# Kernel tuning notes

Measured on AMD Instinct MI355X. Metric: run time of the kernel, lower is better.

The kernel has to match this reference:

```python
import jax, jax.numpy as jnp
import numpy as np


def _ln(z, g, b, eps=1e-5):
    mu = z.mean(-1, keepdims=True)
    v = ((z - mu) ** 2).mean(-1, keepdims=True)
    return (z - mu) / jnp.sqrt(v + eps) * g + b


def _forward(x, C_prev, n_prev, m_prev, ln_in_g, ln_in_b, wq, bq, wk, bk, wv, bv, wi, bi, wf, bf, wo, bo, rd_w1, rd_b1, rd_g, rd_be, rd_w2, rd_b2, ssm_log_lam, ssm_log_b, ssm_c, ssm_log_d, ssm_log_step, ssm_vol_gate, ssm_alpha, ssm_ln_g, ssm_ln_b, ln_mem_g, ln_mem_b):
    B, S, F = x.shape
    D = wq.shape[0]
    sqd = jnp.sqrt(jnp.float32(D))
    w = max(1, int(S * 0.2))
    pad0 = jnp.zeros((B, 1, F), x.dtype)
    cs = jnp.concatenate([pad0, jnp.cumsum(x, 1)], 1)
    cs2 = jnp.concatenate([pad0, jnp.cumsum(x * x, 1)], 1)
    wsum = cs[:, w:] - cs[:, :-w]
    wsq = cs2[:, w:] - cs2[:, :-w]
    var = (wsq - wsum * wsum / w) / (w - 1)
    std = jnp.sqrt(jnp.clip(var, 0.0))
    vol = jnp.concatenate([jnp.broadcast_to(std[:, :1], (B, w - 1, F)), std], 1)
    sv = vol.mean(2, keepdims=True)
    sv = sv / (sv.mean(1, keepdims=True) + 1e-6)  # [B,S,1]
    # --- parallel gate computation ---
    xn = _ln(x, ln_in_g, ln_in_b)
    regime = jax.nn.softmax(jax.nn.gelu(_ln(xn @ rd_w1.T + rd_b1, rd_g, rd_be), approximate=False) @ rd_w2.T + rd_b2, axis=-1)
    q = xn @ wq.T + bq
    k = (xn @ wk.T + bk) / sqd
    v = xn @ wv.T + bv
    it = xn @ wi.T + bi  # [B,S,1]
    ft = xn @ wf.T + bf
    o = jax.nn.sigmoid(xn @ wo.T + bo)
    # --- stabilize_gates (running-max exponential stabilization) ---
    mp = jnp.clip(m_prev, -100.0, 100.0)[:, None, :]  # [B,1,1]
    m_t = jnp.maximum(ft, mp + ft)
    ig = jnp.exp(jnp.clip(it - m_t, -15.0, 15.0))
    fg = jnp.exp(jnp.clip(ft + mp - m_t, -15.0, 15.0))
    # --- store_key_value outer products + cumulative matrix memory ---
    kn = k / (jnp.linalg.norm(k, axis=2, keepdims=True) + 1e-12) * sqd
    vn = v / (jnp.linalg.norm(v, axis=2, keepdims=True) + 1e-6) * sqd
    upd = jnp.clip(ig, 0.0, 1.0)[..., None] * (vn[..., :, None] * kn[..., None, :])  # [B,S,D,D]
    f_cum = jnp.cumprod(fg, axis=1)  # [B,S,1]
    C_t = f_cum[..., None] * C_prev[:, None] + jnp.cumsum(upd, 1)
    # --- structured state-space mixing, vectorized over the D memory rows ---
    lam = -jnp.exp(ssm_log_lam)
    step = jnp.exp(ssm_log_step)
    a_disc = (2.0 + step * lam) / (2.0 - step * lam)  # bilinear discretization
    b_disc = step * (1.0 + a_disc) * jnp.exp(ssm_log_b)[:, 0] / 2.0
    xr = C_t.transpose(0, 2, 1, 3).reshape(B * D, S, D)  # rows folded into batch
    volr = jnp.broadcast_to(sv[:, None, :, 0], (B, D, S)).reshape(B * D, S)
    u = xr.mean(-1)  # [BD,S], per-step scalar drive
    vgate = jax.nn.sigmoid(ssm_vol_gate)
    def stepf(h, inp):
        u_t, vol_t = inp
        h = a_disc[None] * h + b_disc[None] * u_t[:, None]
        h = _ln(h, ssm_ln_g, ssm_ln_b)
        h = h / (1.0 + vgate[None] * vol_t[:, None])
        return h, h
    h0 = jnp.zeros((B * D, D), x.dtype)
    _, hs = jax.lax.scan(stepf, h0, (u.T, volr.T))  # [S,BD,D]
    yscal = jnp.einsum('sbn,n->bs', hs, ssm_c[0])  # [BD,S]
    y = yscal[..., None] + jnp.exp(ssm_log_d) * xr
    alpha = jax.nn.sigmoid(ssm_alpha)
    mixed = alpha * xr + (1.0 - alpha) * y
    C_mixed = mixed.reshape(B, D, S, D).transpose(0, 2, 1, 3)
    mf = regime[:, :, 0:1][..., None]  # regime-aware mixing factor
    C_t = C_mixed * mf + C_t * (1.0 - mf)
    C_t = C_t / (jnp.linalg.norm(C_t.reshape(B, S, D * D), axis=-1)[..., None, None] + 1e-6) * sqd
    # --- mLSTM readout (stabilizer_threshold = 1.0) ---
    n_t = f_cum * n_prev[:, None, :] + jnp.cumsum(ig * k, 1)
    h_til = jnp.einsum('bsij,bsj->bsi', C_t, q)
    denom = jnp.maximum(jnp.abs(jnp.sum(n_t * q, -1, keepdims=True)), 1.0)
    return o * _ln(h_til / denom, ln_mem_g, ln_mem_b)


def setup_inputs() -> dict:
    key = jax.random.key(0)
    ks = jax.random.split(key, 12)
    B, S, F, D = 8, 512, 32, 64
    sF, sD = 1.0 / np.sqrt(F), 1.0 / np.sqrt(D)
    n = lambda k, sh, s=1.0: jax.random.normal(k, sh, jnp.float32) * s
    return dict(
        x=n(ks[0], (B, S, F)),
        C_prev=jnp.zeros((B, D, D), jnp.float32),
        n_prev=jnp.zeros((B, D), jnp.float32),
        m_prev=jnp.zeros((B, 1), jnp.float32),
        ln_in_g=jnp.ones((F,), jnp.float32), ln_in_b=jnp.zeros((F,), jnp.float32),
        wq=n(ks[1], (D, F), sF), bq=jnp.zeros((D,), jnp.float32),
        wk=n(ks[2], (D, F), sF), bk=jnp.zeros((D,), jnp.float32),
        wv=n(ks[3], (D, F), sF), bv=jnp.zeros((D,), jnp.float32),
        wi=n(ks[4], (1, F), sF), bi=jnp.zeros((1,), jnp.float32),
        wf=n(ks[5], (1, F), sF), bf=jnp.ones((1,), jnp.float32),
        wo=n(ks[6], (D, F), sF), bo=jnp.zeros((D,), jnp.float32),
        rd_w1=n(ks[7], (D, F), sF), rd_b1=jnp.zeros((D,), jnp.float32),
        rd_g=jnp.ones((D,), jnp.float32), rd_be=jnp.zeros((D,), jnp.float32),
        rd_w2=n(ks[8], (4, D), sD), rd_b2=jnp.zeros((4,), jnp.float32),
        ssm_log_lam=jnp.linspace(np.log(0.001), np.log(0.1), D).astype(jnp.float32),
        ssm_log_b=jax.random.uniform(ks[9], (D, 1), jnp.float32, -0.5, 0.5),
        ssm_c=n(ks[10], (1, D), sD),
        ssm_log_d=jnp.zeros((1,), jnp.float32),
        ssm_log_step=jnp.float32(np.log(0.001)),
        ssm_vol_gate=jnp.ones((D,), jnp.float32),
        ssm_alpha=jnp.float32(0.7),
        ssm_ln_g=jnp.ones((D,), jnp.float32), ssm_ln_b=jnp.zeros((D,), jnp.float32),
        ln_mem_g=jnp.ones((D,), jnp.float32), ln_mem_b=jnp.zeros((D,), jnp.float32),
    )


def reference(x, C_prev, n_prev, m_prev, ln_in_g, ln_in_b, wq, bq, wk, bk, wv, bv, wi, bi, wf, bf, wo, bo, rd_w1, rd_b1, rd_g, rd_be, rd_w2, rd_b2, ssm_log_lam, ssm_log_b, ssm_c, ssm_log_d, ssm_log_step, ssm_vol_gate, ssm_alpha, ssm_ln_g, ssm_ln_b, ln_mem_g, ln_mem_b):
    return _forward(x, C_prev, n_prev, m_prev, ln_in_g, ln_in_b, wq, bq, wk, bk, wv, bv, wi, bi, wf, bf, wo, bo, rd_w1, rd_b1, rd_g, rd_be, rd_w2, rd_b2, ssm_log_lam, ssm_log_b, ssm_c, ssm_log_d, ssm_log_step, ssm_vol_gate, ssm_alpha, ssm_ln_g, ssm_ln_b, ln_mem_g, ln_mem_b)
```

## Files before the change

### kernel.cpp

```cpp
#include <hip/hip_runtime.h>
#include <math.h>

#define BB 8
#define SS 512
#define FF 32
#define DD 64
#define WVOL 102
#define CH 16
#define NCH (SS / CH)

template<int CTRL, int RM, bool BC>
__device__ __forceinline__ float updpp(float oldv, float x) {
  return __int_as_float(__builtin_amdgcn_update_dpp(
      __float_as_int(oldv), __float_as_int(x), CTRL, RM, 0xF, BC));
}
__device__ __forceinline__ float rlane(float v, int l) {
  return __int_as_float(__builtin_amdgcn_readlane(__float_as_int(v), l));
}
__device__ __forceinline__ float dsum64(float x) {
  x += updpp<0x111, 0xF, true>(0.f, x);
  x += updpp<0x112, 0xF, true>(0.f, x);
  x += updpp<0x114, 0xF, true>(0.f, x);
  x += updpp<0x118, 0xF, true>(0.f, x);
  x += updpp<0x142, 0xF, true>(0.f, x);
  x += updpp<0x143, 0xF, true>(0.f, x);
  return rlane(x, 63);
}
__device__ __forceinline__ void dred2(float& a, float& b) {
  a += updpp<0x111,0xF,true>(0.f,a); b += updpp<0x111,0xF,true>(0.f,b);
  a += updpp<0x112,0xF,true>(0.f,a); b += updpp<0x112,0xF,true>(0.f,b);
  a += updpp<0x114,0xF,true>(0.f,a); b += updpp<0x114,0xF,true>(0.f,b);
  a += updpp<0x118,0xF,true>(0.f,a); b += updpp<0x118,0xF,true>(0.f,b);
  a += updpp<0x142,0xF,true>(0.f,a); b += updpp<0x142,0xF,true>(0.f,b);
  a += updpp<0x143,0xF,true>(0.f,a); b += updpp<0x143,0xF,true>(0.f,b);
  a = rlane(a, 63); b = rlane(b, 63);
}
__device__ __forceinline__ void dred3(float& a, float& b, float& c) {
  a += updpp<0x111,0xF,true>(0.f,a); b += updpp<0x111,0xF,true>(0.f,b); c += updpp<0x111,0xF,true>(0.f,c);
  a += updpp<0x112,0xF,true>(0.f,a); b += updpp<0x112,0xF,true>(0.f,b); c += updpp<0x112,0xF,true>(0.f,c);
  a += updpp<0x114,0xF,true>(0.f,a); b += updpp<0x114,0xF,true>(0.f,b); c += updpp<0x114,0xF,true>(0.f,c);
  a += updpp<0x118,0xF,true>(0.f,a); b += updpp<0x118,0xF,true>(0.f,b); c += updpp<0x118,0xF,true>(0.f,c);
  a += updpp<0x142,0xF,true>(0.f,a); b += updpp<0x142,0xF,true>(0.f,b); c += updpp<0x142,0xF,true>(0.f,c);
  a += updpp<0x143,0xF,true>(0.f,a); b += updpp<0x143,0xF,true>(0.f,b); c += updpp<0x143,0xF,true>(0.f,c);
  a = rlane(a, 63); b = rlane(b, 63); c = rlane(c, 63);
}
__device__ __forceinline__ void dred4(float& a, float& b, float& c, float& d) {
  a += updpp<0x111,0xF,true>(0.f,a); b += updpp<0x111,0xF,true>(0.f,b); c += updpp<0x111,0xF,true>(0.f,c); d += updpp<0x111,0xF,true>(0.f,d);
  a += updpp<0x112,0xF,true>(0.f,a); b += updpp<0x112,0xF,true>(0.f,b); c += updpp<0x112,0xF,true>(0.f,c); d += updpp<0x112,0xF,true>(0.f,d);
  a += updpp<0x114,0xF,true>(0.f,a); b += updpp<0x114,0xF,true>(0.f,b); c += updpp<0x114,0xF,true>(0.f,c); d += updpp<0x114,0xF,true>(0.f,d);
  a += updpp<0x118,0xF,true>(0.f,a); b += updpp<0x118,0xF,true>(0.f,b); c += updpp<0x118,0xF,true>(0.f,c); d += updpp<0x118,0xF,true>(0.f,d);
  a += updpp<0x142,0xF,true>(0.f,a); b += updpp<0x142,0xF,true>(0.f,b); c += updpp<0x142,0xF,true>(0.f,c); d += updpp<0x142,0xF,true>(0.f,d);
  a += updpp<0x143,0xF,true>(0.f,a); b += updpp<0x143,0xF,true>(0.f,b); c += updpp<0x143,0xF,true>(0.f,c); d += updpp<0x143,0xF,true>(0.f,d);
  a = rlane(a, 63); b = rlane(b, 63); c = rlane(c, 63); d = rlane(d, 63);
}
__device__ __forceinline__ void dred2_32(float& a, float& b) {
  a += updpp<0x111,0xF,true>(0.f,a); b += updpp<0x111,0xF,true>(0.f,b);
  a += updpp<0x112,0xF,true>(0.f,a); b += updpp<0x112,0xF,true>(0.f,b);
  a += updpp<0x114,0xF,true>(0.f,a); b += updpp<0x114,0xF,true>(0.f,b);
  a += updpp<0x118,0xF,true>(0.f,a); b += updpp<0x118,0xF,true>(0.f,b);
  a += updpp<0x142,0xF,true>(0.f,a); b += updpp<0x142,0xF,true>(0.f,b);
  a = rlane(a, 31); b = rlane(b, 31);
}
__device__ __forceinline__ float dsum16(float x) {
  x += updpp<0x111, 0xF, true>(0.f, x);
  x += updpp<0x112, 0xF, true>(0.f, x);
  x += updpp<0x114, 0xF, true>(0.f, x);
  x += updpp<0x118, 0xF, true>(0.f, x);
  return x;
}
__device__ __forceinline__ void dscan3(float& f, float& z, float& r) {
  f *= updpp<0x111,0xF,false>(1.f,f); z += updpp<0x111,0xF,true>(0.f,z); r += updpp<0x111,0xF,true>(0.f,r);
  f *= updpp<0x112,0xF,false>(1.f,f); z += updpp<0x112,0xF,true>(0.f,z); r += updpp<0x112,0xF,true>(0.f,r);
  f *= updpp<0x114,0xF,false>(1.f,f); z += updpp<0x114,0xF,true>(0.f,z); r += updpp<0x114,0xF,true>(0.f,r);
  f *= updpp<0x118,0xF,false>(1.f,f); z += updpp<0x118,0xF,true>(0.f,z); r += updpp<0x118,0xF,true>(0.f,r);
  f *= updpp<0x142,0xA,false>(1.f,f); z += updpp<0x142,0xA,true>(0.f,z); r += updpp<0x142,0xA,true>(0.f,r);
  f *= updpp<0x143,0xC,false>(1.f,f); z += updpp<0x143,0xC,true>(0.f,z); r += updpp<0x143,0xC,true>(0.f,r);
}

__global__ void k_prep(const float* __restrict__ Cp,
                       const float* __restrict__ wq, const float* __restrict__ wk,
                       const float* __restrict__ wv, const float* __restrict__ wo,
                       const float* __restrict__ rw1,
                       float* __restrict__ CpT, float* __restrict__ wqT,
                       float* __restrict__ wkT, float* __restrict__ wvT,
                       float* __restrict__ woT, float* __restrict__ rw1T,
                       float* __restrict__ cpr, float* __restrict__ cpn2) {
  int blk = blockIdx.x; int lane = threadIdx.x;
  if (blk < BB) {
    int b = blk;
    const float* rowp = Cp + (size_t)(b * DD + lane) * DD;
    float rs = 0.f, r2 = 0.f;
#pragma unroll 8
    for (int j = 0; j < DD; ++j) {
      float c = rowp[j];
      rs += c; r2 = fmaf(c, c, r2);
      CpT[(size_t)(b * DD + j) * DD + lane] = c;
    }
    cpr[b * DD + lane] = rs;
    float tot2 = dsum64(r2);
    if (lane == 0) cpn2[b] = tot2;
  } else {
    const float* src; float* dst;
    switch (blk - BB) {
      case 0: src = wq;  dst = wqT;  break;
      case 1: src = wk;  dst = wkT;  break;
      case 2: src = wv;  dst = wvT;  break;
      case 3: src = wo;  dst = woT;  break;
      default: src = rw1; dst = rw1T; break;
    }
#pragma unroll 8
    for (int f = 0; f < FF; ++f) dst[f * DD + lane] = src[lane * FF + f];
  }
}

__global__ void k_vol_std(const float* __restrict__ x, float* __restrict__ svraw) {
  int b = blockIdx.x; int s = WVOL - 1 + blockIdx.y;
  int lane = threadIdx.x; int f = lane & 31; int half = lane >> 5;
  const float* xb = x + (size_t)(b * SS) * FF + f;
  float wsum = 0.f, wsq = 0.f;
  int t0 = s - WVOL + 1 + half;
#pragma unroll 17
  for (int k = 0; k < WVOL / 2; ++k) {
    float xv = xb[(t0 + 2 * k) * FF];
    wsum += xv; wsq = fmaf(xv, xv, wsq);
  }
  wsum += __shfl_xor(wsum, 32); wsq += __shfl_xor(wsq, 32);
  float var = (wsq - wsum * wsum * (1.f / WVOL)) * (1.f / (WVOL - 1));
  float sd = sqrtf(fmaxf(var, 0.f));
  float m = dsum64(sd) * 0.5f * (1.f / FF);
  if (lane == 0) svraw[b * SS + s] = m;
}

__global__ void k_proj(const float* __restrict__ x, const float* __restrict__ m_prev,
                       const float* __restrict__ CpT,
                       const float* __restrict__ ln_in_g, const float* __restrict__ ln_in_b,
                       const float* __restrict__ wqT, const float* __restrict__ bq,
                       const float* __restrict__ wkT, const float* __restrict__ bk,
                       const float* __restrict__ wvT, const float* __restrict__ bv,
                       const float* __restrict__ wi, const float* __restrict__ bi,
                       const float* __restrict__ wf, const float* __restrict__ bf,
                       const float* __restrict__ woT, const float* __restrict__ bo,
                       const float* __restrict__ rw1T, const float* __restrict__ rd_b1,
                       const float* __restrict__ rd_g, const float* __restrict__ rd_be,
                       const float* __restrict__ rd_w2, const float* __restrict__ rd_b2,
                       float* __restrict__ qo, float* __restrict__ kno, float* __restrict__ vno,
                       float* __restrict__ iko, float* __restrict__ oo,
                       float* __restrict__ cg_a, float* __restrict__ fg_a,
                       float* __restrict__ mf_a, float* __restrict__ cks_a,
                       float* __restrict__ qsum_a, float* __restrict__ zc) {
  int bs = blockIdx.x; int b = bs / SS;
  int lane = threadIdx.x;
  __shared__ float xs[FF];
  __shared__ float ks[DD];
  float xv = (lane < FF) ? x[bs * FF + lane] : 0.f;
  float s1x = xv, s2x = xv * xv;
  dred2_32(s1x, s2x);
  if (lane < FF) {
    float mu = s1x * (1.f / FF);
    float var = s2x * (1.f / FF) - mu * mu;
    xs[lane] = (xv - mu) * rsqrtf(var + 1e-5f) * ln_in_g[lane] + ln_in_b[lane];
  }
  __syncthreads();
  int d = lane;
  float aq = bq[d], ak = bk[d], av = bv[d], ao = bo[d], at = rd_b1[d];
#pragma unroll
  for (int f = 0; f < FF; ++f) {
    float xf = xs[f];
    aq = fmaf(xf, wqT[f * DD + d], aq);
    ak = fmaf(xf, wkT[f * DD + d], ak);
    av = fmaf(xf, wvT[f * DD + d], av);
    ao = fmaf(xf, woT[f * DD + d], ao);
    at = fmaf(xf, rw1T[f * DD + d], at);
  }
  float pit = (lane < FF) ? xs[lane] * wi[lane] : 0.f;
  float pft = (lane < FF) ? xs[lane] * wf[lane] : 0.f;
  dred2_32(pit, pft);
  float itv = pit + bi[0];
  float ftv = pft + bf[0];
  float s1 = at, s2 = at * at;
  dred2(s1, s2);
  float mu = s1 * (1.f / DD);
  float var = s2 * (1.f / DD) - mu * mu;
  float tn = (at - mu) * rsqrtf(var + 1e-5f) * rd_g[d] + rd_be[d];
  float ge = 0.5f * tn * (1.f + erff(tn * 0.70710678118654752f));
  float l0 = ge * rd_w2[0 * DD + d], l1 = ge * rd_w2[1 * DD + d];
  float l2 = ge * rd_w2[2 * DD + d], l3 = ge * rd_w2[3 * DD + d];
  dred4(l0, l1, l2, l3);
  l0 += rd_b2[0]; l1 += rd_b2[1]; l2 += rd_b2[2]; l3 += rd_b2[3];
  float mx = fmaxf(fmaxf(l0, l1), fmaxf(l2, l3));
  float e0 = expf(l0 - mx), e1 = expf(l1 - mx), e2 = expf(l2 - mx), e3 = expf(l3 - mx);
  float mfv = e0 / (e0 + e1 + e2 + e3);
  float kd = ak * 0.125f;
  float kk = kd * kd, vv = av * av, qsum = aq;
  dred3(kk, vv, qsum);
  float knd = kd * (8.f / (sqrtf(kk) + 1e-12f));
  float vnd = av * (8.f / (sqrtf(vv) + 1e-6f));
  float ksum = dsum64(knd);
  float mp = fminf(fmaxf(m_prev[b], -100.f), 100.f);
  float mt = fmaxf(ftv, mp + ftv);
  float ig = expf(fminf(fmaxf(itv - mt, -15.f), 15.f));
  float fg = expf(fminf(fmaxf(ftv + mp - mt, -15.f), 15.f));
  float cg = fminf(ig, 1.f);
  qo[bs * DD + d] = aq;
  kno[bs * DD + d] = knd;
  vno[bs * DD + d] = vnd;
  iko[bs * DD + d] = ig * kd;
  oo[bs * DD + d] = 1.f / (1.f + expf(-ao));
  ks[d] = knd;
  __syncthreads();
  float acc = 0.f;
  const float* cpt = CpT + (size_t)b * DD * DD;
#pragma unroll 8
  for (int j = 0; j < DD; ++j) acc = fmaf(cpt[j * DD + d], ks[j], acc);
  float z = dsum64(vnd * acc);
  if (lane == 0) {
    cg_a[bs] = cg; fg_a[bs] = fg; mf_a[bs] = mfv;
    cks_a[bs] = cg * ksum; qsum_a[bs] = qsum;
    zc[bs] = cg * z;
  }
}

__global__ void k_qk(const float* __restrict__ qo, const float* __restrict__ kno,
                     const float* __restrict__ vno, const float* __restrict__ cg_a,
                     float* __restrict__ W, float* __restrict__ rho) {
  int blk = blockIdx.x; int b = blk / 136; int r = blk % 136;
  int st = 0;
  while ((st + 1) * (st + 2) / 2 <= r) ++st;
  int tt = r - st * (st + 1) / 2;
  int s0 = st * 32, t0 = tt * 32;
  int tid = threadIdx.x; int ty = tid >> 4, tx = tid & 15;
  __shared__ float qls[32][64], kls[32][64], vsl[32][64];
  __shared__ float ktl[32][68], vtl[32][68];
  __shared__ float cgl[32], sacc[32];
  {
    int col = tid & 63, rg = tid >> 6;
#pragma unroll
    for (int rr = 0; rr < 8; ++rr) {
      int row = rg * 8 + rr;
      int gi = (b * SS + s0 + row) * DD + col;
      int gj = (b * SS + t0 + row) * DD + col;
      qls[row][col] = qo[gi]; kls[row][col] = kno[gi]; vsl[row][col] = vno[gi];
      ktl[row][col] = kno[gj]; vtl[row][col] = vno[gj];
    }
    if (tid < 32) cgl[tid] = cg_a[b * SS + t0 + tid];
  }
  __syncthreads();
  float A[2][2] = {{0.f, 0.f}, {0.f, 0.f}};
  float KK[2][2] = {{0.f, 0.f}, {0.f, 0.f}};
  float VV[2][2] = {{0.f, 0.f}, {0.f, 0.f}};
  for (int k4 = 0; k4 < DD; k4 += 4) {
    float qa[2][4], ka[2][4], va[2][4], kt[2][4], vt[2][4];
#pragma unroll
    for (int i = 0; i < 2; ++i) {
      float4 t1 = *(const float4*)&qls[ty * 2 + i][k4];
      qa[i][0] = t1.x; qa[i][1] = t1.y; qa[i][2] = t1.z; qa[i][3] = t1.w;
      float4 t2 = *(const float4*)&kls[ty * 2 + i][k4];
      ka[i][0] = t2.x; ka[i][1] = t2.y; ka[i][2] = t2.z; ka[i][3] = t2.w;
      float4 t3 = *(const float4*)&vsl[ty * 2 + i][k4];
      va[i][0] = t3.x; va[i][1] = t3.y; va[i][2] = t3.z; va[i][3] = t3.w;
      float4 t4 = *(const float4*)&ktl[tx * 2 + i][k4];
      kt[i][0] = t4.x; kt[i][1] = t4.y; kt[i][2] = t4.z; kt[i][3] = t4.w;
      float4 t5 = *(const float4*)&vtl[tx * 2 + i][k4];
      vt[i][0] = t5.x; vt[i][1] = t5.y; vt[i][2] = t5.z; vt[i][3] = t5.w;
    }
#pragma unroll
    for (int kk = 0; kk < 4; ++kk)
#pragma unroll
      for (int i = 0; i < 2; ++i)
#pragma unroll
        for (int j = 0; j < 2; ++j) {
          A[i][j]  = fmaf(qa[i][kk], kt[j][kk], A[i][j]);
          KK[i][j] = fmaf(ka[i][kk], kt[j][kk], KK[i][j]);
          VV[i][j] = fmaf(va[i][kk], vt[j][kk], VV[i][j]);
        }
  }
  float cg0 = cgl[tx * 2], cg1 = cgl[tx * 2 + 1];
  int tg0 = t0 + tx * 2, tg1 = t0 + tx * 2 + 1;
#pragma unroll
  for (int i = 0; i < 2; ++i) {
    int s = s0 + ty * 2 + i;
    float w0 = (tg0 <= s) ? cg0 * A[i][0] : 0.f;
    float w1 = (tg1 <= s) ? cg1 * A[i][1] : 0.f;
    float2 wst = make_float2(w0, w1);
    *(float2*)&W[((size_t)b * SS + s) * SS + tg0] = wst;
    float wr0 = (tg0 < s) ? 2.f : (tg0 == s ? 1.f : 0.f);
    float wr1 = (tg1 < s) ? 2.f : (tg1 == s ? 1.f : 0.f);
    float rsum = dsum16(fmaf(wr0 * cg0, KK[i][0] * VV[i][0],
                             wr1 * cg1 * KK[i][1] * VV[i][1]));
    if (tx == 15) sacc[ty * 2 + i] = rsum;
  }
  __syncthreads();
  if (tid < 32) {
    int s = s0 + tid;
    atomicAdd(&rho[b * SS + s], cg_a[b * SS + s] * sacc[tid]);
  }
}

__global__ void k_pv(const float* __restrict__ W, const float* __restrict__ vno,
                     float* __restrict__ p2) {
  int blk = blockIdx.x; int b = blk / 26; int u = blk % 26;
  int st32, c0, c1;
  if (u < 6) { st32 = u; c0 = 0; c1 = u >> 1; }
  else {
    int v = u - 6; st32 = 6 + (v >> 1);
    int nch = (st32 >> 1) + 1; int h0 = nch >> 1;
    if (v & 1) { c0 = h0; c1 = nch - 1; } else { c0 = 0; c1 = h0 - 1; }
  }
  int s0 = st32 * 32;
  int tid = threadIdx.x; int ty = tid >> 4, tx = tid & 15;
  __shared__ float wls[32][64];
  __shared__ float vls[64][64];
  float acc[2][4] = {{0.f, 0.f, 0.f, 0.f}, {0.f, 0.f, 0.f, 0.f}};
  for (int c = c0; c <= c1; ++c) {
    __syncthreads();
    int t0 = c * 64;
    int col = tid & 63, rg = tid >> 6;
#pragma unroll
    for (int rr = 0; rr < 8; ++rr) {
      int r2 = rg * 8 + rr;
      wls[r2][col] = W[((size_t)b * SS + s0 + r2) * SS + t0 + col];
    }
#pragma unroll
    for (int rr = 0; rr < 16; ++rr) {
      int t = rg * 16 + rr;
      vls[t][col] = vno[(b * SS + t0 + t) * DD + col];
    }
    __syncthreads();
    for (int k4 = 0; k4 < 64; k4 += 4) {
      float aa[2][4];
#pragma unroll
      for (int i = 0; i < 2; ++i) {
        float4 t1 = *(const float4*)&wls[ty * 2 + i][k4];
        aa[i][0] = t1.x; aa[i][1] = t1.y; aa[i][2] = t1.z; aa[i][3] = t1.w;
      }
      float bb[4][4];
#pragma unroll
      for (int kk = 0; kk < 4; ++kk) {
        float4 t2 = *(const float4*)&vls[k4 + kk][tx * 4];
        bb[kk][0] = t2.x; bb[kk][1] = t2.y; bb[kk][2] = t2.z; bb[kk][3] = t2.w;
      }
#pragma unroll
      for (int kk = 0; kk < 4; ++kk)
#pragma unroll
        for (int i = 0; i < 2; ++i)
#pragma unroll
          for (int j = 0; j < 4; ++j)
            acc[i][j] = fmaf(aa[i][kk], bb[kk][j], acc[i][j]);
    }
  }
#pragma unroll
  for (int i = 0; i < 2; ++i)
#pragma unroll
    for (int j = 0; j < 4; ++j)
      atomicAdd(&p2[(b * SS + s0 + ty * 2 + i) * DD + tx * 4 + j], acc[i][j]);
}

__global__ void k_post(const float* __restrict__ fg_a, const float* __restrict__ zc,
                       const float* __restrict__ rho, const float* __restrict__ svraw,
                       const float* __restrict__ ik, const float* __restrict__ vno,
                       const float* __restrict__ cks_a,
                       float* __restrict__ fcum, float* __restrict__ cpd,
                       float* __restrict__ sn2, float* __restrict__ sv,
                       float* __restrict__ csn, float* __restrict__ csr) {
  int blk = blockIdx.x; int lane = threadIdx.x;
  if (blk < BB) {
    int b = blk;
    float m0 = svraw[b * SS + WVOL - 1];
    float vals[8]; float part = 0.f;
#pragma unroll
    for (int c = 0; c < 8; ++c) {
      int idx = c * 64 + lane;
      float v = (idx < WVOL - 1) ? m0 : svraw[b * SS + idx];
      vals[c] = v; part += v;
    }
    float tot = dsum64(part);
    float inv = 1.f / (tot * (1.f / SS) + 1e-6f);
#pragma unroll
    for (int c = 0; c < 8; ++c) sv[b * SS + c * 64 + lane] = vals[c] * inv;
    float cf = 1.f, cz = 0.f, crr = 0.f;
    for (int c = 0; c < 8; ++c) {
      int bs = b * SS + c * 64 + lane;
      float f = fg_a[bs], z = zc[bs], r = rho[bs];
      dscan3(f, z, r);
      f *= cf; z += cz; r += crr;
      fcum[bs] = f; cpd[bs] = z; sn2[bs] = r;
      cf = rlane(f, 63); cz = rlane(z, 63); crr = rlane(r, 63);
    }
  } else {
    int blk2 = blk - BB; int b = blk2 / NCH; int w = blk2 % NCH; int d = lane;
    float na = 0.f, ra = 0.f;
#pragma unroll
    for (int t = 0; t < CH; ++t) {
      int bs = b * SS + w * CH + t;
      na += ik[bs * DD + d];
      ra = fmaf(cks_a[bs], vno[bs * DD + d], ra);
    }
    csn[blk2 * DD + d] = na; csr[blk2 * DD + d] = ra;
  }
}

__global__ void k_scan_apply(const float* __restrict__ ik, const float* __restrict__ vno,
                             const float* __restrict__ cks_a,
                             const float* __restrict__ csn, const float* __restrict__ csr,
                             const float* __restrict__ sv,
                             const float* __restrict__ cvec, const float* __restrict__ ln_g,
                             const float* __restrict__ ln_b, const float* __restrict__ vol_gate,
                             float* __restrict__ nacc, float* __restrict__ racc,
                             float* __restrict__ S1g, float* __restrict__ S2g) {
  int blk = blockIdx.x;
  if (blk < BB * NCH) {
    int b = blk / NCH; int w = blk % NCH; int d = threadIdx.x;
    float na = 0.f, ra = 0.f;
    for (int w2 = 0; w2 < w; ++w2) {
      na += csn[(b * NCH + w2) * DD + d];
      ra += csr[(b * NCH + w2) * DD + d];
    }
#pragma unroll
    for (int t = 0; t < CH; ++t) {
      int bs = b * SS + w * CH + t;
      na += ik[bs * DD + d];
      ra = fmaf(cks_a[bs], vno[bs * DD + d], ra);
      nacc[bs * DD + d] = na;
      racc[bs * DD + d] = ra;
    }
  } else {
    int bs = blk - BB * NCH;
    int nn = threadIdx.x;
    float cn = cvec[nn], g = ln_g[nn], be = ln_b[nn];
    float vg = 1.f / (1.f + expf(-vol_gate[nn]));
    float vol = sv[bs];
    float rden = __builtin_amdgcn_rcpf(fmaf(vg, vol, 1.f));
    float r1 = cn * g * rden, r2 = cn * be * rden;
    dred2(r1, r2);
    if (nn == 0) { S1g[bs] = r1; S2g[bs] = r2; }
  }
}

__global__ void k_ssm(const float* __restrict__ fcum, const float* __restrict__ racc,
                      const float* __restrict__ cpr, const float* __restrict__ sv,
                      const float* __restrict__ log_lam, const float* __restrict__ log_b,
                      const float* __restrict__ cvec,
                      const float* __restrict__ log_step, const float* __restrict__ vol_gate,
                      const float* __restrict__ ln_g, const float* __restrict__ ln_b,
                      const float* __restrict__ S1g, const float* __restrict__ S2g,
                      float* __restrict__ ysT) {
  int blk = blockIdx.x; int b = blk >> 6; int i = blk & 63;
  int n = threadIdx.x;
  float st = expf(log_step[0]);
  float lam = -expf(log_lam[n]);
  float ad = (2.f + st * lam) / (2.f - st * lam);
  float bd = st * (1.f + ad) * expf(log_b[n]) * 0.5f;
  float vg = 1.f / (1.f + expf(-vol_gate[n]));
  float g = ln_g[n], be = ln_b[n], cn = cvec[n];
  float adg = ad * g, adbe = ad * be, cng = cn * g;
  float cprv = cpr[b * DD + i];
  float u[8], w[8], S1a[8], S2a[8];
#pragma unroll
  for (int c = 0; c < 8; ++c) {
    int s = c * 64 + n; int bs = b * SS + s;
    u[c] = fmaf(fcum[bs], cprv, racc[(size_t)bs * DD + i]) * (1.f / DD);
    w[c] = sv[bs];
    S1a[c] = S1g[bs]; S2a[c] = S2g[bs];
  }
  float ht = bd * rlane(u[0], 0);
#pragma unroll
  for (int c = 0; c < 8; ++c) {
    float macc = 0.f, iacc = 0.f, s3acc = 0.f;
#pragma unroll 4
    for (int t2 = 0; t2 < 64; ++t2) {
      float vvol = rlane(w[c], t2);
      float rden = __builtin_amdgcn_rcpf(fmaf(vg, vvol, 1.f));
      float p1 = ht, p2 = ht * ht, p3 = (cng * rden) * ht;
      p1 += updpp<0x111,0xF,true>(0.f,p1); p2 += updpp<0x111,0xF,true>(0.f,p2); p3 += updpp<0x111,0xF,true>(0.f,p3);
      p1 += updpp<0x112,0xF,true>(0.f,p1); p2 += updpp<0x112,0xF,true>(0.f,p2); p3 += updpp<0x112,0xF,true>(0.f,p3);
      p1 += updpp<0x114,0xF,true>(0.f,p1); p2 += updpp<0x114,0xF,true>(0.f,p2); p3 += updpp<0x114,0xF,true>(0.f,p3);
      p1 += updpp<0x118,0xF,true>(0.f,p1); p2 += updpp<0x118,0xF,true>(0.f,p2); p3 += updpp<0x118,0xF,true>(0.f,p3);
      p1 += updpp<0x142,0xF,true>(0.f,p1); p2 += updpp<0x142,0xF,true>(0.f,p2); p3 += updpp<0x142,0xF,true>(0.f,p3);
      p1 += updpp<0x143,0xF,true>(0.f,p1); p2 += updpp<0x143,0xF,true>(0.f,p2); p3 += updpp<0x143,0xF,true>(0.f,p3);
      float s1 = rlane(p1, 63), s2v = rlane(p2, 63), s3 = rlane(p3, 63);
      float mu = s1 * (1.f / DD);
      float r2m = fmaf(-mu, s1, s2v);
      float arg = fmaxf(fmaf(r2m, 1.f / DD, 1e-5f), 1e-5f);
      float irs = __builtin_amdgcn_rsqf(arg);
      bool sel = (n == t2);
      macc = sel ? mu : macc;
      iacc = sel ? irs : iacc;
      s3acc = sel ? s3 : s3acc;
      float un = (t2 < 63) ? rlane(u[c], t2 + 1)
                           : ((c < 7) ? rlane(u[(c + 1) & 7], 0) : 0.f);
      float A = adg * rden;
      float B = fmaf(adbe, rden, bd * un);
      ht = fmaf((ht - mu) * A, irs, B);
    }
    float y = fmaf(iacc, fmaf(-macc, S1a[c], s3acc), S2a[c]);
    ysT[(size_t)(b * DD + i) * SS + c * 64 + n] = y;
  }
}

__global__ void k_final(const float* __restrict__ qo, const float* __restrict__ oo,
                        const float* __restrict__ p2, const float* __restrict__ racc,
                        const float* __restrict__ nacc, const float* __restrict__ ysT,
                        const float* __restrict__ CpT, const float* __restrict__ cpr,
                        const float* __restrict__ cpn2,
                        const float* __restrict__ fcum, const float* __restrict__ cpd,
                        const float* __restrict__ sn2,
                        const float* __restrict__ mf_a, const float* __restrict__ qsum_a,
                        const float* __restrict__ n_prev,
                        const float* __restrict__ ssm_log_d, const float* __restrict__ ssm_alpha,
                        const float* __restrict__ ln_mem_g, const float* __restrict__ ln_mem_b,
                        float* __restrict__ out) {
  int bs = blockIdx.x; int b = bs / SS; int s = bs % SS;
  int i = threadIdx.x;
  __shared__ float qv[DD];
  float qi = qo[bs * DD + i];
  qv[i] = qi;
  __syncthreads();
  float P1 = 0.f;
  const float* cpt = CpT + (size_t)b * DD * DD;
#pragma unroll 8
  for (int j = 0; j < DD; ++j) P1 = fmaf(cpt[j * DD + i], qv[j], P1);
  float fc = fcum[bs];
  float p = fmaf(fc, P1, p2[bs * DD + i]);
  float r = fmaf(fc, cpr[b * DD + i], racc[bs * DD + i]);
  float R2 = fc * fc * cpn2[b] + 2.f * fc * cpd[bs] + sn2[bs];
  float al = 1.f / (1.f + expf(-ssm_alpha[0]));
  float kap = al + (1.f - al) * expf(ssm_log_d[0]);
  float mfv = mf_a[bs];
  float beta = 1.f + mfv * (kap - 1.f);
  float gam = mfv * (1.f - al);
  float y = ysT[(size_t)(b * DD + i) * SS + s];
  float nt = fmaf(fc, n_prev[b * DD + i], nacc[bs * DD + i]);
  float syr = y * r, sy2 = y * y, ndp = nt * qi;
  dred3(syr, sy2, ndp);
  float nrm2 = fmaxf(beta * beta * R2 + 2.f * beta * gam * syr + gam * gam * (float)DD * sy2, 0.f);
  float scale = 8.f / (sqrtf(nrm2) + 1e-6f);
  float denom = fmaxf(fabsf(ndp), 1.f);
  float hh = scale * (fmaf(beta, p, gam * y * qsum_a[bs])) / denom;
  float s1 = hh, s2 = hh * hh;
  dred2(s1, s2);
  float mu = s1 * (1.f / DD);
  float var = fmaxf(s2 * (1.f / DD) - mu * mu, 0.f);
  float o = (hh - mu) * rsqrtf(var + 1e-5f) * ln_mem_g[i] + ln_mem_b[i];
  out[bs * DD + i] = oo[bs * DD + i] * o;
}

extern "C" void kernel_launch(void* const* d_in, const int* in_sizes, int n_in,
                              void* d_out, int out_size, void* d_ws, size_t ws_size,
                              hipStream_t stream) {
  const float* x        = (const float*)d_in[0];
  const float* C_prev   = (const float*)d_in[1];
  const float* n_prev   = (const float*)d_in[2];
  const float* m_prev   = (const float*)d_in[3];
  const float* ln_in_g  = (const float*)d_in[4];
  const float* ln_in_b  = (const float*)d_in[5];
  const float* wq = (const float*)d_in[6];  const float* bq = (const float*)d_in[7];
  const float* wk = (const float*)d_in[8];  const float* bk = (const float*)d_in[9];
  const float* wv = (const float*)d_in[10]; const float* bv = (const float*)d_in[11];
  const float* wi = (const float*)d_in[12]; const float* bi = (const float*)d_in[13];
  const float* wf = (const float*)d_in[14]; const float* bf = (const float*)d_in[15];
  const float* wo = (const float*)d_in[16]; const float* bo = (const float*)d_in[17];
  const float* rd_w1 = (const float*)d_in[18]; const float* rd_b1 = (const float*)d_in[19];
  const float* rd_g  = (const float*)d_in[20]; const float* rd_be = (const float*)d_in[21];
  const float* rd_w2 = (const float*)d_in[22]; const float* rd_b2 = (const float*)d_in[23];
  const float* ssm_log_lam  = (const float*)d_in[24];
  const float* ssm_log_b    = (const float*)d_in[25];
  const float* ssm_c        = (const float*)d_in[26];
  const float* ssm_log_d    = (const float*)d_in[27];
  const float* ssm_log_step = (const float*)d_in[28];
  const float* ssm_vol_gate = (const float*)d_in[29];
  const float* ssm_alpha    = (const float*)d_in[30];
  const float* ssm_ln_g     = (const float*)d_in[31];
  const float* ssm_ln_b     = (const float*)d_in[32];
  const float* ln_mem_g     = (const float*)d_in[33];
  const float* ln_mem_b     = (const float*)d_in[34];
  float* out = (float*)d_out;

  float* Wsp = (float*)d_ws;
  size_t o0 = 0;
  const size_t BS = (size_t)BB * SS, BSD = BS * DD, WSZ = (size_t)BB * SS * SS;
  float* sv    = Wsp + o0; o0 += BS;
  float* svraw = Wsp + o0; o0 += BS;
  float* qo   = Wsp + o0; o0 += BSD;
  float* kno  = Wsp + o0; o0 += BSD;
  float* vno  = Wsp + o0; o0 += BSD;
  float* iko  = Wsp + o0; o0 += BSD;
  float* oo   = Wsp + o0; o0 += BSD;
  float* racc = Wsp + o0; o0 += BSD;
  float* nacc = Wsp + o0; o0 += BSD;
  float* ysT  = Wsp + o0; o0 += BSD;
  float* p2   = Wsp + o0; o0 += BSD;
  float* rho  = Wsp + o0; o0 += BS;
  float* Wm   = Wsp + o0; o0 += WSZ;
  float* cg_a = Wsp + o0; o0 += BS;
  float* fg_a = Wsp + o0; o0 += BS;
  float* mf_a = Wsp + o0; o0 += BS;
  float* cks  = Wsp + o0; o0 += BS;
  float* qsum = Wsp + o0; o0 += BS;
  float* zc   = Wsp + o0; o0 += BS;
  float* fcum = Wsp + o0; o0 += BS;
  float* cpd  = Wsp + o0; o0 += BS;
  float* sn2  = Wsp + o0; o0 += BS;
  float* S1g  = Wsp + o0; o0 += BS;
  float* S2g  = Wsp + o0; o0 += BS;
  float* cpr  = Wsp + o0; o0 += (size_t)BB * DD;
  float* cpn2 = Wsp + o0; o0 += BB;
  float* csn  = Wsp + o0; o0 += (size_t)BB * NCH * DD;
  float* csr  = Wsp + o0; o0 += (size_t)BB * NCH * DD;
  float* CpT  = Wsp + o0; o0 += (size_t)BB * DD * DD;
  float* wqT  = Wsp + o0; o0 += (size_t)FF * DD;
  float* wkT  = Wsp + o0; o0 += (size_t)FF * DD;
  float* wvT  = Wsp + o0; o0 += (size_t)FF * DD;
  float* woT  = Wsp + o0; o0 += (size_t)FF * DD;
  float* rw1T = Wsp + o0; o0 += (size_t)FF * DD;

  hipMemsetAsync(p2, 0, (BSD + BS + WSZ) * sizeof(float), stream);
  hipLaunchKernelGGL(k_prep, dim3(BB + 5), dim3(64), 0, stream,
                     C_prev, wq, wk, wv, wo, rd_w1,
                     CpT, wqT, wkT, wvT, woT, rw1T, cpr, cpn2);
  hipLaunchKernelGGL(k_vol_std, dim3(BB, SS - WVOL + 1), dim3(64), 0, stream, x, svraw);
  hipLaunchKernelGGL(k_proj, dim3(BB * SS), dim3(64), 0, stream,
                     x, m_prev, CpT, ln_in_g, ln_in_b, wqT, bq, wkT, bk, wvT, bv, wi, bi,
                     wf, bf, woT, bo, rw1T, rd_b1, rd_g, rd_be, rd_w2, rd_b2,
                     qo, kno, vno, iko, oo, cg_a, fg_a, mf_a, cks, qsum, zc);
  hipLaunchKernelGGL(k_qk, dim3(BB * 136), dim3(256), 0, stream,
                     qo, kno, vno, cg_a, Wm, rho);
  hipLaunchKernelGGL(k_pv, dim3(BB * 26), dim3(256), 0, stream, Wm, vno, p2);
  hipLaunchKernelGGL(k_post, dim3(BB + BB * NCH), dim3(64), 0, stream,
                     fg_a, zc, rho, svraw, iko, vno, cks,
                     fcum, cpd, sn2, sv, csn, csr);
  hipLaunchKernelGGL(k_scan_apply, dim3(BB * NCH + BB * SS), dim3(64), 0, stream,
                     iko, vno, cks, csn, csr, sv, ssm_c, ssm_ln_g, ssm_ln_b,
                     ssm_vol_gate, nacc, racc, S1g, S2g);
  hipLaunchKernelGGL(k_ssm, dim3(BB * DD), dim3(64), 0, stream,
                     fcum, racc, cpr, sv, ssm_log_lam, ssm_log_b, ssm_c,
                     ssm_log_step, ssm_vol_gate, ssm_ln_g, ssm_ln_b, S1g, S2g, ysT);
  hipLaunchKernelGGL(k_final, dim3(BB * SS), dim3(64), 0, stream,
                     qo, oo, p2, racc, nacc, ysT, CpT, cpr, cpn2, fcum, cpd, sn2,
                     mf_a, qsum, n_prev, ssm_log_d, ssm_alpha, ln_mem_g, ln_mem_b, out);
}
```

Measured before the change: 300.4 us.

## Pack four SSM rows per wave and precompute per-step gate coefficients

The SSM scan kernel now processes four memory rows per 64-lane wave, with 16 lanes per row and four state elements per lane. The per-step LayerNorm reductions therefore need only four in-row DPP steps instead of a full-wave reduction plus readlanes. The per-step volatility-dependent coefficients (ad*g/rden, ad*be/rden, c*g/rden) are precomputed in the scan_apply kernel into three new B×S×D buffers. The scan reads them as float4, prefetched one step ahead. This shortens the serial dependency chain per step and raises per-lane ILP. In exchange it launches a quarter as many waves, adds global traffic for the coefficient buffers, and puts dependent global loads inside the sequential loop.

```diff
diff --git a/kernel.cpp b/kernel.cpp
--- a/kernel.cpp
+++ b/kernel.cpp
@@ -405,8 +405,11 @@
                              const float* __restrict__ sv,
                              const float* __restrict__ cvec, const float* __restrict__ ln_g,
                              const float* __restrict__ ln_b, const float* __restrict__ vol_gate,
+                             const float* __restrict__ log_lam, const float* __restrict__ log_step,
                              float* __restrict__ nacc, float* __restrict__ racc,
-                             float* __restrict__ S1g, float* __restrict__ S2g) {
+                             float* __restrict__ S1g, float* __restrict__ S2g,
+                             float* __restrict__ AdgR, float* __restrict__ AbeR,
+                             float* __restrict__ CngR) {
   int blk = blockIdx.x;
   if (blk < BB * NCH) {
     int b = blk / NCH; int w = blk % NCH; int d = threadIdx.x;
@@ -428,72 +431,128 @@
     int nn = threadIdx.x;
     float cn = cvec[nn], g = ln_g[nn], be = ln_b[nn];
     float vg = 1.f / (1.f + expf(-vol_gate[nn]));
+    float st = expf(log_step[0]);
+    float lam = -expf(log_lam[nn]);
+    float ad = (2.f + st * lam) / (2.f - st * lam);
     float vol = sv[bs];
     float rden = __builtin_amdgcn_rcpf(fmaf(vg, vol, 1.f));
-    float r1 = cn * g * rden, r2 = cn * be * rden;
+    float cgr = cn * g * rden;
+    AdgR[(size_t)bs * DD + nn] = ad * g * rden;
+    AbeR[(size_t)bs * DD + nn] = ad * be * rden;
+    CngR[(size_t)bs * DD + nn] = cgr;
+    float r1 = cgr, r2 = cn * be * rden;
     dred2(r1, r2);
     if (nn == 0) { S1g[bs] = r1; S2g[bs] = r2; }
   }
 }
 
 __global__ void k_ssm(const float* __restrict__ fcum, const float* __restrict__ racc,
-                      const float* __restrict__ cpr, const float* __restrict__ sv,
+                      const float* __restrict__ cpr,
+                      const float* __restrict__ AdgR, const float* __restrict__ AbeR,
+                      const float* __restrict__ CngR,
+                      const float* __restrict__ S1g, const float* __restrict__ S2g,
                       const float* __restrict__ log_lam, const float* __restrict__ log_b,
-                      const float* __restrict__ cvec,
-                      const float* __restrict__ log_step, const float* __restrict__ vol_gate,
-                      const float* __restrict__ ln_g, const float* __restrict__ ln_b,
-                      const float* __restrict__ S1g, const float* __restrict__ S2g,
+                      const float* __restrict__ log_step,
                       float* __restrict__ ysT) {
-  int blk = blockIdx.x; int b = blk >> 6; int i = blk & 63;
-  int n = threadIdx.x;
+  int w = blockIdx.x;
+  int b = w >> 4;
+  int ig = (w & 15) << 2;
+  int lane = threadIdx.x;
+  int n16 = lane & 15, row = lane >> 4;
   float st = expf(log_step[0]);
-  float lam = -expf(log_lam[n]);
-  float ad = (2.f + st * lam) / (2.f - st * lam);
-  float bd = st * (1.f + ad) * expf(log_b[n]) * 0.5f;
-  float vg = 1.f / (1.f + expf(-vol_gate[n]));
-  float g = ln_g[n], be = ln_b[n], cn = cvec[n];
-  float adg = ad * g, adbe = ad * be, cng = cn * g;
-  float cprv = cpr[b * DD + i];
-  float u[8], w[8], S1a[8], S2a[8];
-#pragma unroll
+  float bd4[4];
+#pragma unroll
+  for (int k = 0; k < 4; ++k) {
+    int n = 4 * n16 + k;
+    float lam = -expf(log_lam[n]);
+    float ad = (2.f + st * lam) / (2.f - st * lam);
+    bd4[k] = st * (1.f + ad) * expf(log_b[n]) * 0.5f;
+  }
+  __shared__ float uL[4][65];
+  int si = lane & 3, tl = lane >> 2;
+  float cprv = cpr[b * DD + ig + si];
+  const size_t tbase = (size_t)b * SS * DD + 4 * n16;
+  const float* Ap = AdgR + tbase;
+  const float* Bp = AbeR + tbase;
+  const float* Pp = CngR + tbase;
+#pragma unroll
+  for (int p = 0; p < 4; ++p) {
+    int t = p * 16 + tl;
+    int bs = b * SS + t;
+    uL[si][t] = fmaf(fcum[bs], cprv, racc[(size_t)bs * DD + ig + si]) * (1.f / DD);
+  }
+  if (lane < 4) {
+    int bs = b * SS + 64;
+    uL[lane][64] = fmaf(fcum[bs], cpr[b * DD + ig + lane],
+                        racc[(size_t)bs * DD + ig + lane]) * (1.f / DD);
+  }
+  __syncthreads();
+  float u0 = uL[row][0];
+  float h0 = bd4[0] * u0, h1 = bd4[1] * u0, h2 = bd4[2] * u0, h3 = bd4[3] * u0;
+  float4 a4 = *(const float4*)Ap;
+  float4 b4 = *(const float4*)Bp;
+  float4 p4 = *(const float4*)Pp;
   for (int c = 0; c < 8; ++c) {
-    int s = c * 64 + n; int bs = b * SS + s;
-    u[c] = fmaf(fcum[bs], cprv, racc[(size_t)bs * DD + i]) * (1.f / DD);
-    w[c] = sv[bs];
-    S1a[c] = S1g[bs]; S2a[c] = S2g[bs];
-  }
-  float ht = bd * rlane(u[0], 0);
-#pragma unroll
-  for (int c = 0; c < 8; ++c) {
-    float macc = 0.f, iacc = 0.f, s3acc = 0.f;
-#pragma unroll 4
-    for (int t2 = 0; t2 < 64; ++t2) {
-      float vvol = rlane(w[c], t2);
-      float rden = __builtin_amdgcn_rcpf(fmaf(vg, vvol, 1.f));
-      float p1 = ht, p2 = ht * ht, p3 = (cng * rden) * ht;
-      p1 += updpp<0x111,0xF,true>(0.f,p1); p2 += updpp<0x111,0xF,true>(0.f,p2); p3 += updpp<0x111,0xF,true>(0.f,p3);
-      p1 += updpp<0x112,0xF,true>(0.f,p1); p2 += updpp<0x112,0xF,true>(0.f,p2); p3 += updpp<0x112,0xF,true>(0.f,p3);
-      p1 += updpp<0x114,0xF,true>(0.f,p1); p2 += updpp<0x114,0xF,true>(0.f,p2); p3 += updpp<0x114,0xF,true>(0.f,p3);
-      p1 += updpp<0x118,0xF,true>(0.f,p1); p2 += updpp<0x118,0xF,true>(0.f,p2); p3 += updpp<0x118,0xF,true>(0.f,p3);
-      p1 += updpp<0x142,0xF,true>(0.f,p1); p2 += updpp<0x142,0xF,true>(0.f,p2); p3 += updpp<0x142,0xF,true>(0.f,p3);
-      p1 += updpp<0x143,0xF,true>(0.f,p1); p2 += updpp<0x143,0xF,true>(0.f,p2); p3 += updpp<0x143,0xF,true>(0.f,p3);
-      float s1 = rlane(p1, 63), s2v = rlane(p2, 63), s3 = rlane(p3, 63);
-      float mu = s1 * (1.f / DD);
-      float r2m = fmaf(-mu, s1, s2v);
-      float arg = fmaxf(fmaf(r2m, 1.f / DD, 1e-5f), 1e-5f);
-      float irs = __builtin_amdgcn_rsqf(arg);
-      bool sel = (n == t2);
-      macc = sel ? mu : macc;
-      iacc = sel ? irs : iacc;
-      s3acc = sel ? s3 : s3acc;
-      float un = (t2 < 63) ? rlane(u[c], t2 + 1)
-                           : ((c < 7) ? rlane(u[(c + 1) & 7], 0) : 0.f);
-      float A = adg * rden;
-      float B = fmaf(adbe, rden, bd * un);
-      ht = fmaf((ht - mu) * A, irs, B);
-    }
-    float y = fmaf(iacc, fmaf(-macc, S1a[c], s3acc), S2a[c]);
-    ysT[(size_t)(b * DD + i) * SS + c * 64 + n] = y;
+    if (c) {
+      __syncthreads();
+#pragma unroll
+      for (int p = 0; p < 4; ++p) {
+        int t = c * 64 + p * 16 + tl;
+        int bs = b * SS + t;
+        uL[si][p * 16 + tl] = fmaf(fcum[bs], cprv, racc[(size_t)bs * DD + ig + si]) * (1.f / DD);
+      }
+      if (lane < 4) {
+        int t = c * 64 + 64;
+        float uu = 0.f;
+        if (t < SS) {
+          int bs = b * SS + t;
+          uu = fmaf(fcum[bs], cpr[b * DD + ig + lane],
+                    racc[(size_t)bs * DD + ig + lane]) * (1.f / DD);
+        }
+        uL[lane][64] = uu;
+      }
+      __syncthreads();
+    }
+    for (int q = 0; q < 4; ++q) {
+      float macc = 0.f, iacc = 0.f, s3acc = 0.f;
+#pragma unroll
+      for (int tt = 0; tt < 16; ++tt) {
+        int t = c * 64 + q * 16 + tt;
+        float4 a4n = *(const float4*)(Ap + (size_t)(t + 1) * DD);
+        float4 b4n = *(const float4*)(Bp + (size_t)(t + 1) * DD);
+        float4 p4n = *(const float4*)(Pp + (size_t)(t + 1) * DD);
+        float un = uL[row][q * 16 + tt + 1];
+        float s1 = (h0 + h1) + (h2 + h3);
+        float s2 = fmaf(h0, h0, h1 * h1) + fmaf(h2, h2, h3 * h3);
+        float s3 = fmaf(p4.x, h0, p4.y * h1) + fmaf(p4.z, h2, p4.w * h3);
+        s1 += updpp<0xB1,0xF,true>(0.f,s1); s2 += updpp<0xB1,0xF,true>(0.f,s2); s3 += updpp<0xB1,0xF,true>(0.f,s3);
+        s1 += updpp<0x4E,0xF,true>(0.f,s1); s2 += updpp<0x4E,0xF,true>(0.f,s2); s3 += updpp<0x4E,0xF,true>(0.f,s3);
+        s1 += updpp<0x141,0xF,true>(0.f,s1); s2 += updpp<0x141,0xF,true>(0.f,s2); s3 += updpp<0x141,0xF,true>(0.f,s3);
+        s1 += updpp<0x140,0xF,true>(0.f,s1); s2 += updpp<0x140,0xF,true>(0.f,s2); s3 += updpp<0x140,0xF,true>(0.f,s3);
+        float mu = s1 * (1.f / DD);
+        float r2m = fmaf(-mu, s1, s2);
+        float arg = fmaxf(fmaf(r2m, 1.f / DD, 1e-5f), 1e-5f);
+        float irs = __builtin_amdgcn_rsqf(arg);
+        bool sel = (n16 == tt);
+        macc = sel ? mu : macc;
+        iacc = sel ? irs : iacc;
+        s3acc = sel ? s3 : s3acc;
+        float m2 = mu * irs;
+        float bo0 = fmaf(bd4[0], un, b4.x);
+        float bo1 = fmaf(bd4[1], un, b4.y);
+        float bo2 = fmaf(bd4[2], un, b4.z);
+        float bo3 = fmaf(bd4[3], un, b4.w);
+        h0 = fmaf(h0, irs * a4.x, fmaf(-m2, a4.x, bo0));
+        h1 = fmaf(h1, irs * a4.y, fmaf(-m2, a4.y, bo1));
+        h2 = fmaf(h2, irs * a4.z, fmaf(-m2, a4.z, bo2));
+        h3 = fmaf(h3, irs * a4.w, fmaf(-m2, a4.w, bo3));
+        a4 = a4n; b4 = b4n; p4 = p4n;
+      }
+      int tf = c * 64 + q * 16 + n16;
+      float S1v = S1g[b * SS + tf], S2v = S2g[b * SS + tf];
+      float y = fmaf(iacc, fmaf(-macc, S1v, s3acc), S2v);
+      ysT[(size_t)(b * DD + ig + row) * SS + tf] = y;
+    }
   }
 }
 
@@ -588,6 +647,9 @@
   float* racc = Wsp + o0; o0 += BSD;
   float* nacc = Wsp + o0; o0 += BSD;
   float* ysT  = Wsp + o0; o0 += BSD;
+  float* AdgR = Wsp + o0; o0 += BSD;
+  float* AbeR = Wsp + o0; o0 += BSD;
+  float* CngR = Wsp + o0; o0 += BSD;
   float* p2   = Wsp + o0; o0 += BSD;
   float* rho  = Wsp + o0; o0 += BS;
   float* Wm   = Wsp + o0; o0 += WSZ;
@@ -630,10 +692,11 @@
                      fcum, cpd, sn2, sv, csn, csr);
   hipLaunchKernelGGL(k_scan_apply, dim3(BB * NCH + BB * SS), dim3(64), 0, stream,
                      iko, vno, cks, csn, csr, sv, ssm_c, ssm_ln_g, ssm_ln_b,
-                     ssm_vol_gate, nacc, racc, S1g, S2g);
-  hipLaunchKernelGGL(k_ssm, dim3(BB * DD), dim3(64), 0, stream,
-                     fcum, racc, cpr, sv, ssm_log_lam, ssm_log_b, ssm_c,
-                     ssm_log_step, ssm_vol_gate, ssm_ln_g, ssm_ln_b, S1g, S2g, ysT);
+                     ssm_vol_gate, ssm_log_lam, ssm_log_step,
+                     nacc, racc, S1g, S2g, AdgR, AbeR, CngR);
+  hipLaunchKernelGGL(k_ssm, dim3(BB * 16), dim3(64), 0, stream,
+                     fcum, racc, cpr, AdgR, AbeR, CngR, S1g, S2g,
+                     ssm_log_lam, ssm_log_b, ssm_log_step, ysT);
   hipLaunchKernelGGL(k_final, dim3(BB * SS), dim3(64), 0, stream,
                      qo, oo, p2, racc, nacc, ysT, CpT, cpr, cpn2, fcum, cpd, sn2,
                      mf_a, qsum, n_prev, ssm_log_d, ssm_alpha, ln_mem_g, ln_mem_b, out);
```

Result: slower. 442.5 us (+47.3%).
